# Performance work log

Hardware: AMD Instinct MI355X
Metric: run time of the kernel (lower is better)

The kernel has to match this reference:

```python
import jax, jax.numpy as jnp
import numpy as np

N_NODES = 50000
N_EDGES = 800000
D_IN, D_LAT, D_EMB = 512, 256, 64
NEG_SLOPE = 0.2


def segment_softmax(logits, seg, num_segments):
    # numerically stable softmax over variable-size neighborhoods grouped by seg
    m = jax.ops.segment_max(logits, seg, num_segments=num_segments)
    e = jnp.exp(logits - m[seg])
    s = jax.ops.segment_sum(e, seg, num_segments=num_segments)
    return e / s[seg]


def setup_inputs() -> dict:
    key = jax.random.key(0)
    k = jax.random.split(key, 6)
    x = jax.random.normal(k[0], (N_NODES, D_IN), dtype=jnp.float32)
    graph_edges = jax.random.randint(k[1], (2, N_EDGES), 0, N_NODES, dtype=jnp.int32)
    # learned parameters (glorot-ish scaling)
    W1 = jax.random.normal(k[2], (D_IN, D_LAT), dtype=jnp.float32) / np.sqrt(D_IN)
    a1_src = jax.random.normal(k[3], (D_LAT,), dtype=jnp.float32) / np.sqrt(D_LAT)
    a1_dst = jax.random.normal(k[4], (D_LAT,), dtype=jnp.float32) / np.sqrt(D_LAT)
    W2 = jax.random.normal(k[5], (D_LAT, D_EMB), dtype=jnp.float32) / np.sqrt(D_LAT)
    return {"x": x, "W1": W1, "a1_src": a1_src, "a1_dst": a1_dst, "W2": W2,
            "graph_edges": graph_edges}


def reference(x, W1, a1_src, a1_dst, W2, graph_edges):
    src = graph_edges[0]  # message source j
    dst = graph_edges[1]  # aggregation target i
    n = x.shape[0]

    # --- encoder layer 1 (full GAT, heads=1, no bias, no self loops) ---
    h1 = x @ W1                                   # [N, D_LAT]
    als = h1 @ a1_src                             # [N] per-node src logits
    ald = h1 @ a1_dst                             # [N] per-node dst logits
    e1 = jax.nn.leaky_relu(als[src] + ald[dst], NEG_SLOPE)   # [E]
    alpha1 = segment_softmax(e1, dst, n)          # [E]
    agg1 = jax.ops.segment_sum(alpha1[:, None] * h1[src], dst, num_segments=n)
    inter = jax.nn.elu(agg1)                      # [N, D_LAT]

    # --- encoder layer 2 (compute_attention=False -> plain linear) ---
    emb = inter @ W2                              # [N, D_EMB]

    # --- decoder layer 1 (weights tied to W2^T, attention tied to layer1) ---
    h3 = emb @ W2.T                               # [N, D_LAT]
    # tied attention: reuse layer1's per-node logits (als, ald)
    e3 = jax.nn.leaky_relu(als[src] + ald[dst], NEG_SLOPE)
    alpha3 = segment_softmax(e3, dst, n)
    agg3 = jax.ops.segment_sum(alpha3[:, None] * h3[src], dst, num_segments=n)
    dec_inter = jax.nn.elu(agg3)                  # [N, D_LAT]

    # --- decoder layer 2 (compute_attention=False -> plain linear, W1^T) ---
    recon = dec_inter @ W1.T                      # [N, D_IN]
    return emb, recon
```

## Files before the change

kernel.cpp:

```cpp
#include <hip/hip_runtime.h>
#include <math.h>

#define N_NODES 50000
#define N_EDGES 800000
#define D_IN 512
#define D_LAT 256
#define D_EMB 64
#define NEG_SLOPE 0.2f

typedef __attribute__((ext_vector_type(8))) short bf16x8;
typedef __attribute__((ext_vector_type(8))) unsigned short u16x8;
typedef __attribute__((ext_vector_type(4))) float f32x4;

__device__ __forceinline__ ushort f2b(float f) {
  union { float f; unsigned u; } v; v.f = f;
  return (ushort)((v.u + 0x7fffu + ((v.u >> 16) & 1u)) >> 16);
}
__device__ __forceinline__ float b2f(ushort h) {
  union { unsigned u; float f; } v; v.u = ((unsigned)h) << 16;
  return v.f;
}

__device__ __forceinline__ float wave_reduce_sum(float v) {
#pragma unroll
  for (int off = 32; off > 0; off >>= 1) v += __shfl_xor(v, off, 64);
  return v;
}

template <int BM, int BN, int WR, int WC, int AF32, int WF32, int WBF16,
          int ELU, int LOGIT>
__global__ __launch_bounds__(WR * WC * 64) void gemm_mfma(
    const void* __restrict__ Aptr, const ushort* __restrict__ B,
    float* __restrict__ Cf, ushort* __restrict__ Cb, int M, int N, int K,
    const float* __restrict__ a_src, const float* __restrict__ a_dst,
    float* __restrict__ als, float* __restrict__ ald) {
  constexpr int BK = 32;
  constexpr int WTM = BM / WR, WTN = BN / WC;
  constexpr int FM = WTM / 16, FN = WTN / 16;
  constexpr int NT = WR * WC * 64;
  constexpr int AIT = (BM * BK * 2) / (NT * 16);
  constexpr int BIT_ = (BN * BK * 2) / (NT * 16);
  __shared__ ushort As[BM][BK];
  __shared__ ushort Bs[BN][BK];
  const int tid = threadIdx.x, lane = tid & 63, wid = tid >> 6;
  const int wr = wid / WC, wc = wid % WC;
  const int bm = blockIdx.y * BM, bn = blockIdx.x * BN;
  f32x4 acc[FM][FN] = {};

  for (int k0 = 0; k0 < K; k0 += BK) {
    if constexpr (AF32) {
      const float* Af = (const float*)Aptr;
#pragma unroll
      for (int it = 0; it < AIT; ++it) {
        int off = it * (NT * 16) + tid * 16;
        int row = off >> 6;
        int ecol = (off & 63) >> 1;
        int grow = bm + row; grow = grow < M ? grow : (M - 1);
        const float* g = Af + (size_t)grow * K + k0 + ecol;
        float4 f0 = *(const float4*)g;
        float4 f1 = *(const float4*)(g + 4);
        u16x8 hb;
        hb[0] = f2b(f0.x); hb[1] = f2b(f0.y); hb[2] = f2b(f0.z); hb[3] = f2b(f0.w);
        hb[4] = f2b(f1.x); hb[5] = f2b(f1.y); hb[6] = f2b(f1.z); hb[7] = f2b(f1.w);
        *(u16x8*)((char*)&As[0][0] + off) = hb;
      }
    } else {
      const ushort* Ab = (const ushort*)Aptr;
#pragma unroll
      for (int it = 0; it < AIT; ++it) {
        int off = it * (NT * 16) + tid * 16;
        int row = off >> 6;
        int grow = bm + row; grow = grow < M ? grow : (M - 1);
        const ushort* g = Ab + (size_t)grow * K + k0 + ((off & 63) >> 1);
        __builtin_amdgcn_global_load_lds(
            (const __attribute__((address_space(1))) void*)g,
            (__attribute__((address_space(3))) void*)((char*)&As[0][0] + off),
            16, 0, 0);
      }
    }
#pragma unroll
    for (int it = 0; it < BIT_; ++it) {
      int off = it * (NT * 16) + tid * 16;
      int row = off >> 6;
      const ushort* g = B + (size_t)(bn + row) * K + k0 + ((off & 63) >> 1);
      __builtin_amdgcn_global_load_lds(
          (const __attribute__((address_space(1))) void*)g,
          (__attribute__((address_space(3))) void*)((char*)&Bs[0][0] + off),
          16, 0, 0);
    }
    __syncthreads();
    const int kb = (lane >> 4) * 8, rl = lane & 15;
    bf16x8 af[FM], bfr[FN];
#pragma unroll
    for (int i = 0; i < FM; ++i)
      af[i] = *(const bf16x8*)&As[wr * WTM + i * 16 + rl][kb];
#pragma unroll
    for (int j = 0; j < FN; ++j)
      bfr[j] = *(const bf16x8*)&Bs[wc * WTN + j * 16 + rl][kb];
#pragma unroll
    for (int i = 0; i < FM; ++i)
#pragma unroll
      for (int j = 0; j < FN; ++j)
        acc[i][j] = __builtin_amdgcn_mfma_f32_16x16x32_bf16(af[i], bfr[j],
                                                            acc[i][j], 0, 0, 0);
    __syncthreads();
  }
  const int cl = lane & 15, rg = (lane >> 4) * 4;
#pragma unroll
  for (int i = 0; i < FM; ++i)
#pragma unroll
    for (int j = 0; j < FN; ++j)
#pragma unroll
      for (int r = 0; r < 4; ++r) {
        int grow = bm + wr * WTM + i * 16 + rg + r;
        if (grow >= M) continue;
        int gcol = bn + wc * WTN + j * 16 + cl;
        float v = acc[i][j][r];
        if (ELU) v = v > 0.f ? v : __expf(v) - 1.f;
        if (WF32) Cf[(size_t)grow * N + gcol] = v;
        if (WBF16) Cb[(size_t)grow * N + gcol] = f2b(v);
      }
  if constexpr (LOGIT) {
    __shared__ float alsP[BM], aldP[BM];
    for (int t = tid; t < BM; t += NT) { alsP[t] = 0.f; aldP[t] = 0.f; }
    __syncthreads();
    float asv[FN], adv[FN];
#pragma unroll
    for (int j = 0; j < FN; ++j) {
      int col = bn + wc * WTN + j * 16 + cl;
      asv[j] = a_src[col];
      adv[j] = a_dst[col];
    }
#pragma unroll
    for (int i = 0; i < FM; ++i)
#pragma unroll
      for (int r = 0; r < 4; ++r) {
        float s = 0.f, d = 0.f;
#pragma unroll
        for (int j = 0; j < FN; ++j) {
          s += acc[i][j][r] * asv[j];
          d += acc[i][j][r] * adv[j];
        }
#pragma unroll
        for (int off = 1; off < 16; off <<= 1) {
          s += __shfl_xor(s, off, 64);
          d += __shfl_xor(d, off, 64);
        }
        if (cl == 0) {
          int row = wr * WTM + i * 16 + rg + r;
          atomicAdd(&alsP[row], s);
          atomicAdd(&aldP[row], d);
        }
      }
    __syncthreads();
    for (int t = tid; t < BM; t += NT) {
      int gr = bm + t;
      if (gr < M) { als[gr] = alsP[t]; ald[gr] = aldP[t]; }
    }
  }
}

__global__ __launch_bounds__(256) void conv_weights_hist(
    const float* __restrict__ W1, const float* __restrict__ W2,
    ushort* __restrict__ W1b, ushort* __restrict__ W1tb,
    ushort* __restrict__ W2b, ushort* __restrict__ W2tb,
    const int* __restrict__ dst, int* __restrict__ counts) {
  int i = blockIdx.x * blockDim.x + threadIdx.x;
  if (i < D_IN * D_LAT) {
    ushort b = f2b(W1[i]);
    int r = i / D_LAT, c = i % D_LAT;
    W1b[i] = b;
    W1tb[(size_t)c * D_IN + r] = b;
  }
  if (i < D_LAT * D_EMB) {
    ushort b = f2b(W2[i]);
    int r = i / D_EMB, c = i % D_EMB;
    W2b[i] = b;
    W2tb[(size_t)c * D_LAT + r] = b;
  }
  if (i < N_EDGES) atomicAdd(&counts[dst[i]], 1);
}

#define SCAN_NBLK ((N_NODES + 511) / 512)

__global__ __launch_bounds__(512) void scan_phase1(
    const int* __restrict__ counts, int* __restrict__ rowptr,
    int* __restrict__ bsum) {
  __shared__ int wsum[9];
  int idx = blockIdx.x * 512 + threadIdx.x;
  int lane = threadIdx.x & 63, wv = threadIdx.x >> 6;
  int c = (idx < N_NODES) ? counts[idx] : 0;
  int v = c;
#pragma unroll
  for (int off = 1; off < 64; off <<= 1) {
    int t = __shfl_up(v, off, 64);
    if (lane >= off) v += t;
  }
  if (lane == 63) wsum[wv] = v;
  __syncthreads();
  if (threadIdx.x == 0) {
    int r = 0;
    for (int i = 0; i < 8; i++) { int t = wsum[i]; wsum[i] = r; r += t; }
    bsum[blockIdx.x] = r;
  }
  __syncthreads();
  if (idx < N_NODES) rowptr[idx] = wsum[wv] + v - c;
}

__global__ __launch_bounds__(128) void scan_phase2(int* __restrict__ bsum) {
  __shared__ int s[128];
  int tid = threadIdx.x;
  int v = (tid < SCAN_NBLK) ? bsum[tid] : 0;
  s[tid] = v;
  __syncthreads();
  for (int off = 1; off < 128; off <<= 1) {
    int t = (tid >= off) ? s[tid - off] : 0;
    __syncthreads();
    s[tid] += t;
    __syncthreads();
  }
  if (tid < SCAN_NBLK) bsum[tid] = s[tid] - v;
}

__device__ __forceinline__ int grp(const int* rowptr, const int* bsum,
                                   int idx) {
  return rowptr[idx] + bsum[idx >> 9];
}
__device__ __forceinline__ int grp_end(const int* rowptr, const int* bsum,
                                       int node) {
  return (node + 1 < N_NODES) ? rowptr[node + 1] + bsum[(node + 1) >> 9]
                              : N_EDGES;
}

__global__ void scatter_kernel(const int* __restrict__ src,
                               const int* __restrict__ dst,
                               const float* __restrict__ als,
                               const float* __restrict__ ald,
                               const int* __restrict__ rowptr,
                               const int* __restrict__ bsum,
                               int* __restrict__ fill, int* __restrict__ ssrc,
                               float* __restrict__ slogit) {
  int e = blockIdx.x * blockDim.x + threadIdx.x;
  if (e >= N_EDGES) return;
  int s = src[e], d = dst[e];
  int pos = grp(rowptr, bsum, d) + atomicAdd(&fill[d], 1);
  float x = als[s] + ald[d];
  slogit[pos] = (x > 0.f) ? x : NEG_SLOPE * x;
  ssrc[pos] = s;
}

__global__ __launch_bounds__(256) void agg_bf16_sm(
    const ushort* __restrict__ feat, const int* __restrict__ rowptr,
    const int* __restrict__ bsum, const int* __restrict__ ssrc,
    const float* __restrict__ slogit, float* __restrict__ alphaE,
    float* __restrict__ invOut, ushort* __restrict__ out) {
  int wave = threadIdx.x >> 6, lane = threadIdx.x & 63;
  int node = blockIdx.x * 4 + wave;
  if (node >= N_NODES) return;
  int beg = grp(rowptr, bsum, node), end = grp_end(rowptr, bsum, node);
  float s = 0.f;
  for (int e = beg + lane; e < end; e += 64) {
    float ev = __expf(slogit[e]);
    alphaE[e] = ev;
    s += ev;
  }
  s = wave_reduce_sum(s);
  float inv = (s > 0.f) ? 1.f / s : 0.f;
  if (lane == 0) invOut[node] = inv;

  int half = lane >> 5, hl = lane & 31;
  float acc[8] = {};
  int e = beg + half;
  for (; e + 6 < end; e += 8) {
    int s0 = ssrc[e], s1 = ssrc[e + 2], s2 = ssrc[e + 4], s3 = ssrc[e + 6];
    float e0 = __expf(slogit[e]);
    float e1 = __expf(slogit[e + 2]);
    float e2 = __expf(slogit[e + 4]);
    float e3 = __expf(slogit[e + 6]);
    u16x8 h0 = *(const u16x8*)(feat + (size_t)s0 * D_LAT + hl * 8);
    u16x8 h1 = *(const u16x8*)(feat + (size_t)s1 * D_LAT + hl * 8);
    u16x8 h2 = *(const u16x8*)(feat + (size_t)s2 * D_LAT + hl * 8);
    u16x8 h3 = *(const u16x8*)(feat + (size_t)s3 * D_LAT + hl * 8);
#pragma unroll
    for (int q = 0; q < 8; q++) acc[q] += e0 * b2f(h0[q]);
#pragma unroll
    for (int q = 0; q < 8; q++) acc[q] += e1 * b2f(h1[q]);
#pragma unroll
    for (int q = 0; q < 8; q++) acc[q] += e2 * b2f(h2[q]);
#pragma unroll
    for (int q = 0; q < 8; q++) acc[q] += e3 * b2f(h3[q]);
  }
  for (; e < end; e += 2) {
    float ev = __expf(slogit[e]);
    int s2 = ssrc[e];
    u16x8 h = *(const u16x8*)(feat + (size_t)s2 * D_LAT + hl * 8);
#pragma unroll
    for (int q = 0; q < 8; q++) acc[q] += ev * b2f(h[q]);
  }
#pragma unroll
  for (int q = 0; q < 8; q++) acc[q] += __shfl_xor(acc[q], 32, 64);
  if (half == 0) {
    u16x8 o;
#pragma unroll
    for (int q = 0; q < 8; q++) {
      float v = acc[q] * inv;
      o[q] = f2b(v > 0.f ? v : __expf(v) - 1.f);
    }
    *(u16x8*)(out + (size_t)node * D_LAT + hl * 8) = o;
  }
}

__global__ __launch_bounds__(256) void agg_emb(
    const ushort* __restrict__ feat, const int* __restrict__ rowptr,
    const int* __restrict__ bsum, const int* __restrict__ ssrc,
    const float* __restrict__ alphaE, const float* __restrict__ invArr,
    ushort* __restrict__ out) {
  int wave = threadIdx.x >> 6, lane = threadIdx.x & 63;
  int node = blockIdx.x * 4 + wave;
  if (node >= N_NODES) return;
  int beg = grp(rowptr, bsum, node), end = grp_end(rowptr, bsum, node);
  int q = lane >> 4, ql = lane & 15;
  float acc[4] = {};
  int e = beg + q;
  for (; e + 4 < end; e += 8) {
    float a0 = alphaE[e], a1 = alphaE[e + 4];
    int s0 = ssrc[e], s1 = ssrc[e + 4];
    ushort4 h0 = *(const ushort4*)(feat + (size_t)s0 * D_EMB + ql * 4);
    ushort4 h1 = *(const ushort4*)(feat + (size_t)s1 * D_EMB + ql * 4);
    acc[0] += a0 * b2f(h0.x) + a1 * b2f(h1.x);
    acc[1] += a0 * b2f(h0.y) + a1 * b2f(h1.y);
    acc[2] += a0 * b2f(h0.z) + a1 * b2f(h1.z);
    acc[3] += a0 * b2f(h0.w) + a1 * b2f(h1.w);
  }
  for (; e < end; e += 4) {
    float a = alphaE[e];
    int s = ssrc[e];
    ushort4 h = *(const ushort4*)(feat + (size_t)s * D_EMB + ql * 4);
    acc[0] += a * b2f(h.x);
    acc[1] += a * b2f(h.y);
    acc[2] += a * b2f(h.z);
    acc[3] += a * b2f(h.w);
  }
#pragma unroll
  for (int k = 0; k < 4; k++) {
    acc[k] += __shfl_xor(acc[k], 16, 64);
    acc[k] += __shfl_xor(acc[k], 32, 64);
  }
  if (q == 0) {
    float inv = invArr[node];
    ushort4 o;
    o.x = f2b(acc[0] * inv); o.y = f2b(acc[1] * inv);
    o.z = f2b(acc[2] * inv); o.w = f2b(acc[3] * inv);
    *(ushort4*)(out + (size_t)node * D_EMB + ql * 4) = o;
  }
}

extern "C" void kernel_launch(void* const* d_in, const int* in_sizes, int n_in,
                              void* d_out, int out_size, void* d_ws,
                              size_t ws_size, hipStream_t stream) {
  const float* x = (const float*)d_in[0];
  const float* W1 = (const float*)d_in[1];
  const float* a1s = (const float*)d_in[2];
  const float* a1d = (const float*)d_in[3];
  const float* W2 = (const float*)d_in[4];
  const int* ge = (const int*)d_in[5];
  const int* esrc = ge;
  const int* edst = ge + N_EDGES;

  float* out = (float*)d_out;
  float* emb = out;
  float* recon = out + (size_t)N_NODES * D_EMB;

  char* w = (char*)d_ws;
  ushort* h1b = (ushort*)w;    w += (size_t)N_NODES * D_LAT * 2;
  ushort* interb = (ushort*)w; w += (size_t)N_NODES * D_LAT * 2;
  ushort* embb = (ushort*)w;   w += (size_t)N_NODES * D_EMB * 2;
  ushort* W1b = (ushort*)w;    w += (size_t)D_IN * D_LAT * 2;
  ushort* W1tb = (ushort*)w;   w += (size_t)D_LAT * D_IN * 2;
  ushort* W2b = (ushort*)w;    w += (size_t)D_LAT * D_EMB * 2;
  ushort* W2tb = (ushort*)w;   w += (size_t)D_EMB * D_LAT * 2;
  float* als = (float*)w;      w += (size_t)N_NODES * 4;
  float* ald = (float*)w;      w += (size_t)N_NODES * 4;
  int* counts = (int*)w;       w += (size_t)N_NODES * 4;
  int* fill = (int*)w;         w += (size_t)N_NODES * 4;
  int* rowptr = (int*)w;       w += (size_t)(N_NODES + 4) * 4;
  int* bsum = (int*)w;         w += 128 * 4;
  int* ssrc = (int*)w;         w += (size_t)N_EDGES * 4;
  float* slogit = (float*)w;   w += (size_t)N_EDGES * 4;
  float* alphaE = (float*)w;   w += (size_t)N_EDGES * 4;

  hipMemsetAsync(counts, 0, (size_t)N_NODES * 8, stream);

  dim3 b256(256), b512(512);
  const int MB = (N_NODES + 127) / 128;

  conv_weights_hist<<<(N_EDGES + 255) / 256, b256, 0, stream>>>(
      W1, W2, W1b, W1tb, W2b, W2tb, edst, counts);

  gemm_mfma<128, 256, 2, 4, 1, 0, 1, 0, 1><<<dim3(1, MB), b512, 0, stream>>>(
      x, W1tb, (float*)nullptr, h1b, N_NODES, D_LAT, D_IN, a1s, a1d, als, ald);
  scan_phase1<<<SCAN_NBLK, 512, 0, stream>>>(counts, rowptr, bsum);
  scan_phase2<<<1, 128, 0, stream>>>(bsum);
  scatter_kernel<<<(N_EDGES + 255) / 256, b256, 0, stream>>>(
      esrc, edst, als, ald, rowptr, bsum, fill, ssrc, slogit);
  float* invArr = ald;
  agg_bf16_sm<<<(N_NODES + 3) / 4, b256, 0, stream>>>(
      h1b, rowptr, bsum, ssrc, slogit, alphaE, invArr, interb);
  gemm_mfma<128, 64, 2, 2, 0, 1, 1, 0, 0><<<dim3(1, MB), b256, 0, stream>>>(
      interb, W2tb, emb, embb, N_NODES, D_EMB, D_LAT, nullptr, nullptr,
      nullptr, nullptr);
  ushort* aggEb = interb;
  agg_emb<<<(N_NODES + 3) / 4, b256, 0, stream>>>(embb, rowptr, bsum, ssrc,
                                                  alphaE, invArr, aggEb);
  ushort* decb = h1b;
  gemm_mfma<128, 256, 2, 4, 0, 0, 1, 1, 0><<<dim3(1, MB), b512, 0, stream>>>(
      aggEb, W2b, (float*)nullptr, decb, N_NODES, D_LAT, D_EMB, nullptr,
      nullptr, nullptr, nullptr);
  gemm_mfma<128, 256, 2, 4, 0, 1, 0, 0, 0><<<dim3(D_IN / 256, MB), b512, 0,
                                              stream>>>(
      decb, W1b, recon, (ushort*)nullptr, N_NODES, D_IN, D_LAT, nullptr,
      nullptr, nullptr, nullptr);
}
```

Baseline: 279.7 us.

## Fuse decoder aggregation with W2 GEMM and use chained single-pass scan

Replaces the two-kernel block scan with a single decoupled-lookback chained scan that writes absolute row pointers, which removes the bsum indirection from every consumer. The stored alphaE array is dropped, and the exp weights are recomputed from slogit wherever they are needed. The decoder edge aggregation over 64-dim embeddings is fused with the 64→256 GEMM and ELU into one kernel that keeps the aggregated tile in swizzled LDS, removing a launch and an intermediate global round trip. The costs are a serialized spin-wait between scan blocks, and 16 serial node aggregations per wave in the fused kernel, which may limit parallelism.

```diff
diff --git a/kernel.cpp b/kernel.cpp
--- a/kernel.cpp
+++ b/kernel.cpp
@@ -183,10 +183,11 @@
 
 #define SCAN_NBLK ((N_NODES + 511) / 512)
 
-__global__ __launch_bounds__(512) void scan_phase1(
+__global__ __launch_bounds__(512) void scan_chained(
     const int* __restrict__ counts, int* __restrict__ rowptr,
-    int* __restrict__ bsum) {
+    int* __restrict__ pf) {
   __shared__ int wsum[9];
+  __shared__ int sprefix;
   int idx = blockIdx.x * 512 + threadIdx.x;
   int lane = threadIdx.x & 63, wv = threadIdx.x >> 6;
   int c = (idx < N_NODES) ? counts[idx] : 0;
@@ -201,35 +202,21 @@
   if (threadIdx.x == 0) {
     int r = 0;
     for (int i = 0; i < 8; i++) { int t = wsum[i]; wsum[i] = r; r += t; }
-    bsum[blockIdx.x] = r;
+    int prev = 0;
+    if (blockIdx.x > 0) {
+      int f;
+      do { f = atomicAdd(&pf[blockIdx.x - 1], 0); } while (!(f & 0x40000000));
+      prev = f & 0x3fffffff;
+    }
+    atomicExch(&pf[blockIdx.x], 0x40000000 | (prev + r));
+    sprefix = prev;
   }
   __syncthreads();
-  if (idx < N_NODES) rowptr[idx] = wsum[wv] + v - c;
-}
-
-__global__ __launch_bounds__(128) void scan_phase2(int* __restrict__ bsum) {
-  __shared__ int s[128];
-  int tid = threadIdx.x;
-  int v = (tid < SCAN_NBLK) ? bsum[tid] : 0;
-  s[tid] = v;
-  __syncthreads();
-  for (int off = 1; off < 128; off <<= 1) {
-    int t = (tid >= off) ? s[tid - off] : 0;
-    __syncthreads();
-    s[tid] += t;
-    __syncthreads();
-  }
-  if (tid < SCAN_NBLK) bsum[tid] = s[tid] - v;
-}
-
-__device__ __forceinline__ int grp(const int* rowptr, const int* bsum,
-                                   int idx) {
-  return rowptr[idx] + bsum[idx >> 9];
-}
-__device__ __forceinline__ int grp_end(const int* rowptr, const int* bsum,
-                                       int node) {
-  return (node + 1 < N_NODES) ? rowptr[node + 1] + bsum[(node + 1) >> 9]
-                              : N_EDGES;
+  if (idx < N_NODES) rowptr[idx] = sprefix + wsum[wv] + v - c;
+}
+
+__device__ __forceinline__ int seg_end(const int* rowptr, int node) {
+  return (node + 1 < N_NODES) ? rowptr[node + 1] : N_EDGES;
 }
 
 __global__ void scatter_kernel(const int* __restrict__ src,
@@ -237,13 +224,12 @@
                                const float* __restrict__ als,
                                const float* __restrict__ ald,
                                const int* __restrict__ rowptr,
-                               const int* __restrict__ bsum,
                                int* __restrict__ fill, int* __restrict__ ssrc,
                                float* __restrict__ slogit) {
   int e = blockIdx.x * blockDim.x + threadIdx.x;
   if (e >= N_EDGES) return;
   int s = src[e], d = dst[e];
-  int pos = grp(rowptr, bsum, d) + atomicAdd(&fill[d], 1);
+  int pos = rowptr[d] + atomicAdd(&fill[d], 1);
   float x = als[s] + ald[d];
   slogit[pos] = (x > 0.f) ? x : NEG_SLOPE * x;
   ssrc[pos] = s;
@@ -251,19 +237,14 @@
 
 __global__ __launch_bounds__(256) void agg_bf16_sm(
     const ushort* __restrict__ feat, const int* __restrict__ rowptr,
-    const int* __restrict__ bsum, const int* __restrict__ ssrc,
-    const float* __restrict__ slogit, float* __restrict__ alphaE,
+    const int* __restrict__ ssrc, const float* __restrict__ slogit,
     float* __restrict__ invOut, ushort* __restrict__ out) {
   int wave = threadIdx.x >> 6, lane = threadIdx.x & 63;
   int node = blockIdx.x * 4 + wave;
   if (node >= N_NODES) return;
-  int beg = grp(rowptr, bsum, node), end = grp_end(rowptr, bsum, node);
+  int beg = rowptr[node], end = seg_end(rowptr, node);
   float s = 0.f;
-  for (int e = beg + lane; e < end; e += 64) {
-    float ev = __expf(slogit[e]);
-    alphaE[e] = ev;
-    s += ev;
-  }
+  for (int e = beg + lane; e < end; e += 64) s += __expf(slogit[e]);
   s = wave_reduce_sum(s);
   float inv = (s > 0.f) ? 1.f / s : 0.f;
   if (lane == 0) invOut[node] = inv;
@@ -310,49 +291,103 @@
   }
 }
 
-__global__ __launch_bounds__(256) void agg_emb(
-    const ushort* __restrict__ feat, const int* __restrict__ rowptr,
-    const int* __restrict__ bsum, const int* __restrict__ ssrc,
-    const float* __restrict__ alphaE, const float* __restrict__ invArr,
-    ushort* __restrict__ out) {
-  int wave = threadIdx.x >> 6, lane = threadIdx.x & 63;
-  int node = blockIdx.x * 4 + wave;
-  if (node >= N_NODES) return;
-  int beg = grp(rowptr, bsum, node), end = grp_end(rowptr, bsum, node);
-  int q = lane >> 4, ql = lane & 15;
-  float acc[4] = {};
-  int e = beg + q;
-  for (; e + 4 < end; e += 8) {
-    float a0 = alphaE[e], a1 = alphaE[e + 4];
-    int s0 = ssrc[e], s1 = ssrc[e + 4];
-    ushort4 h0 = *(const ushort4*)(feat + (size_t)s0 * D_EMB + ql * 4);
-    ushort4 h1 = *(const ushort4*)(feat + (size_t)s1 * D_EMB + ql * 4);
-    acc[0] += a0 * b2f(h0.x) + a1 * b2f(h1.x);
-    acc[1] += a0 * b2f(h0.y) + a1 * b2f(h1.y);
-    acc[2] += a0 * b2f(h0.z) + a1 * b2f(h1.z);
-    acc[3] += a0 * b2f(h0.w) + a1 * b2f(h1.w);
-  }
-  for (; e < end; e += 4) {
-    float a = alphaE[e];
-    int s = ssrc[e];
-    ushort4 h = *(const ushort4*)(feat + (size_t)s * D_EMB + ql * 4);
-    acc[0] += a * b2f(h.x);
-    acc[1] += a * b2f(h.y);
-    acc[2] += a * b2f(h.z);
-    acc[3] += a * b2f(h.w);
-  }
-#pragma unroll
-  for (int k = 0; k < 4; k++) {
-    acc[k] += __shfl_xor(acc[k], 16, 64);
-    acc[k] += __shfl_xor(acc[k], 32, 64);
-  }
-  if (q == 0) {
-    float inv = invArr[node];
-    ushort4 o;
-    o.x = f2b(acc[0] * inv); o.y = f2b(acc[1] * inv);
-    o.z = f2b(acc[2] * inv); o.w = f2b(acc[3] * inv);
-    *(ushort4*)(out + (size_t)node * D_EMB + ql * 4) = o;
-  }
+__global__ __launch_bounds__(512) void dec_fused(
+    const ushort* __restrict__ embb, const int* __restrict__ rowptr,
+    const int* __restrict__ ssrc, const float* __restrict__ slogit,
+    const float* __restrict__ invArr, const ushort* __restrict__ W2b,
+    ushort* __restrict__ decb, int M) {
+  __shared__ ushort aggL[128 * 64];
+  __shared__ ushort Bs[256][32];
+  const int tid = threadIdx.x, lane = tid & 63, wid = tid >> 6;
+  const int bm = blockIdx.x * 128;
+  const int q = lane >> 4, ql = lane & 15;
+  for (int t = 0; t < 16; ++t) {
+    int ln = wid * 16 + t;
+    int gn = bm + ln;
+    float a0 = 0.f, a1 = 0.f, a2 = 0.f, a3 = 0.f;
+    if (gn < N_NODES) {
+      int beg = rowptr[gn], end = seg_end(rowptr, gn);
+      int e = beg + q;
+      for (; e + 4 < end; e += 8) {
+        float w0 = __expf(slogit[e]), w1 = __expf(slogit[e + 4]);
+        int s0 = ssrc[e], s1 = ssrc[e + 4];
+        ushort4 h0 = *(const ushort4*)(embb + (size_t)s0 * D_EMB + ql * 4);
+        ushort4 h1 = *(const ushort4*)(embb + (size_t)s1 * D_EMB + ql * 4);
+        a0 += w0 * b2f(h0.x) + w1 * b2f(h1.x);
+        a1 += w0 * b2f(h0.y) + w1 * b2f(h1.y);
+        a2 += w0 * b2f(h0.z) + w1 * b2f(h1.z);
+        a3 += w0 * b2f(h0.w) + w1 * b2f(h1.w);
+      }
+      for (; e < end; e += 4) {
+        float wv = __expf(slogit[e]);
+        int s0 = ssrc[e];
+        ushort4 h = *(const ushort4*)(embb + (size_t)s0 * D_EMB + ql * 4);
+        a0 += wv * b2f(h.x);
+        a1 += wv * b2f(h.y);
+        a2 += wv * b2f(h.z);
+        a3 += wv * b2f(h.w);
+      }
+    }
+    a0 += __shfl_xor(a0, 16, 64); a0 += __shfl_xor(a0, 32, 64);
+    a1 += __shfl_xor(a1, 16, 64); a1 += __shfl_xor(a1, 32, 64);
+    a2 += __shfl_xor(a2, 16, 64); a2 += __shfl_xor(a2, 32, 64);
+    a3 += __shfl_xor(a3, 16, 64); a3 += __shfl_xor(a3, 32, 64);
+    if (q == 0) {
+      float inv = (gn < N_NODES) ? invArr[gn] : 0.f;
+      ushort4 o;
+      o.x = f2b(a0 * inv); o.y = f2b(a1 * inv);
+      o.z = f2b(a2 * inv); o.w = f2b(a3 * inv);
+      int byte = (ln * 128 + ql * 8) ^ ((ln & 7) << 4);
+      *(ushort4*)((char*)aggL + byte) = o;
+    }
+  }
+  const int wr = wid / 4, wc = wid % 4;
+  f32x4 acc[4][4] = {};
+  const int kb = (lane >> 4) * 8, rl = lane & 15;
+  for (int k0 = 0; k0 < 64; k0 += 32) {
+#pragma unroll
+    for (int it = 0; it < 2; ++it) {
+      int off = it * 8192 + tid * 16;
+      int row = off >> 6;
+      const ushort* g = W2b + (size_t)row * 64 + k0 + ((off & 63) >> 1);
+      __builtin_amdgcn_global_load_lds(
+          (const __attribute__((address_space(1))) void*)g,
+          (__attribute__((address_space(3))) void*)((char*)&Bs[0][0] + off),
+          16, 0, 0);
+    }
+    __syncthreads();
+    bf16x8 af[4], bfr[4];
+#pragma unroll
+    for (int i = 0; i < 4; ++i) {
+      int row = wr * 64 + i * 16 + rl;
+      int byte = (row * 128 + (k0 + kb) * 2) ^ ((row & 7) << 4);
+      af[i] = *(const bf16x8*)((char*)aggL + byte);
+    }
+#pragma unroll
+    for (int j = 0; j < 4; ++j)
+      bfr[j] = *(const bf16x8*)&Bs[wc * 64 + j * 16 + rl][kb];
+#pragma unroll
+    for (int i = 0; i < 4; ++i)
+#pragma unroll
+      for (int j = 0; j < 4; ++j)
+        acc[i][j] = __builtin_amdgcn_mfma_f32_16x16x32_bf16(af[i], bfr[j],
+                                                            acc[i][j], 0, 0, 0);
+    __syncthreads();
+  }
+  const int cl = lane & 15, rg = (lane >> 4) * 4;
+#pragma unroll
+  for (int i = 0; i < 4; ++i)
+#pragma unroll
+    for (int j = 0; j < 4; ++j)
+#pragma unroll
+      for (int r = 0; r < 4; ++r) {
+        int grow = bm + wr * 64 + i * 16 + rg + r;
+        if (grow >= M) continue;
+        int gcol = wc * 64 + j * 16 + cl;
+        float v = acc[i][j][r];
+        v = v > 0.f ? v : __expf(v) - 1.f;
+        decb[(size_t)grow * D_LAT + gcol] = f2b(v);
+      }
 }
 
 extern "C" void kernel_launch(void* const* d_in, const int* in_sizes, int n_in,
@@ -383,39 +418,32 @@
   float* ald = (float*)w;      w += (size_t)N_NODES * 4;
   int* counts = (int*)w;       w += (size_t)N_NODES * 4;
   int* fill = (int*)w;         w += (size_t)N_NODES * 4;
+  int* pf = (int*)w;           w += 128 * 4;
   int* rowptr = (int*)w;       w += (size_t)(N_NODES + 4) * 4;
-  int* bsum = (int*)w;         w += 128 * 4;
   int* ssrc = (int*)w;         w += (size_t)N_EDGES * 4;
   float* slogit = (float*)w;   w += (size_t)N_EDGES * 4;
-  float* alphaE = (float*)w;   w += (size_t)N_EDGES * 4;
-
-  hipMemsetAsync(counts, 0, (size_t)N_NODES * 8, stream);
+
+  hipMemsetAsync(counts, 0, (size_t)N_NODES * 8 + 128 * 4, stream);
 
   dim3 b256(256), b512(512);
   const int MB = (N_NODES + 127) / 128;
 
   conv_weights_hist<<<(N_EDGES + 255) / 256, b256, 0, stream>>>(
       W1, W2, W1b, W1tb, W2b, W2tb, edst, counts);
-
   gemm_mfma<128, 256, 2, 4, 1, 0, 1, 0, 1><<<dim3(1, MB), b512, 0, stream>>>(
       x, W1tb, (float*)nullptr, h1b, N_NODES, D_LAT, D_IN, a1s, a1d, als, ald);
-  scan_phase1<<<SCAN_NBLK, 512, 0, stream>>>(counts, rowptr, bsum);
-  scan_phase2<<<1, 128, 0, stream>>>(bsum);
+  scan_chained<<<SCAN_NBLK, b512, 0, stream>>>(counts, rowptr, pf);
   scatter_kernel<<<(N_EDGES + 255) / 256, b256, 0, stream>>>(
-      esrc, edst, als, ald, rowptr, bsum, fill, ssrc, slogit);
+      esrc, edst, als, ald, rowptr, fill, ssrc, slogit);
   float* invArr = ald;
   agg_bf16_sm<<<(N_NODES + 3) / 4, b256, 0, stream>>>(
-      h1b, rowptr, bsum, ssrc, slogit, alphaE, invArr, interb);
+      h1b, rowptr, ssrc, slogit, invArr, interb);
   gemm_mfma<128, 64, 2, 2, 0, 1, 1, 0, 0><<<dim3(1, MB), b256, 0, stream>>>(
       interb, W2tb, emb, embb, N_NODES, D_EMB, D_LAT, nullptr, nullptr,
       nullptr, nullptr);
-  ushort* aggEb = interb;
-  agg_emb<<<(N_NODES + 3) / 4, b256, 0, stream>>>(embb, rowptr, bsum, ssrc,
-                                                  alphaE, invArr, aggEb);
   ushort* decb = h1b;
-  gemm_mfma<128, 256, 2, 4, 0, 0, 1, 1, 0><<<dim3(1, MB), b512, 0, stream>>>(
-      aggEb, W2b, (float*)nullptr, decb, N_NODES, D_LAT, D_EMB, nullptr,
-      nullptr, nullptr, nullptr);
+  dec_fused<<<MB, b512, 0, stream>>>(embb, rowptr, ssrc, slogit, invArr, W2b,
+                                     decb, N_NODES);
   gemm_mfma<128, 256, 2, 4, 0, 1, 0, 0, 0><<<dim3(D_IN / 256, MB), b512, 0,
                                               stream>>>(
       decb, W1b, recon, (ushort*)nullptr, N_NODES, D_IN, D_LAT, nullptr,
```

Result: slower. 347.7 us (+24.3%).
